# Optimization experiments

Hardware: AMD Instinct MI355X
Metric: run time of the kernel (lower is better)

## Reference

```python
import jax, jax.numpy as jnp
import numpy as np

T, H_IN = 2048, 84
HID = 256
NA = 18


def _conv(x, w, b, stride):
    # x: [N,C,H,W], w: [O,I,kh,kw]
    y = jax.lax.conv_general_dilated(
        x, w, window_strides=(stride, stride), padding='VALID',
        dimension_numbers=('NCHW', 'OIHW', 'NCHW'))
    return jax.nn.relu(y + b[None, :, None, None])


def setup_inputs() -> dict:
    key = jax.random.key(0)
    ks = jax.random.split(key, 17)
    p = lambda k, shape, s=0.05: (jax.random.normal(k, shape, jnp.float32) * s)
    return {
        'input_frames': jax.random.uniform(ks[0], (T, 1, H_IN, H_IN), jnp.float32),
        'conv1_w': p(ks[1], (32, 1, 8, 8)),   'conv1_b': p(ks[2], (32,)),
        'conv2_w': p(ks[3], (64, 32, 4, 4)),  'conv2_b': p(ks[4], (64,)),
        'conv3_w': p(ks[5], (256, 64, 3, 3)), 'conv3_b': p(ks[6], (256,)),
        'attn_w1': p(ks[7], (HID, HID)),      'attn_b1': p(ks[8], (HID,)),
        'attn_w2': p(ks[9], (HID, HID)),      'attn_b2': p(ks[10], (HID,)),
        'lstm_w_ih': p(ks[11], (4 * HID, HID)), 'lstm_w_hh': p(ks[12], (4 * HID, HID)),
        'lstm_b_ih': p(ks[13], (4 * HID,)),     'lstm_b_hh': p(ks[14], (4 * HID,)),
        'q_w': p(ks[15], (NA, HID)),          'q_b': p(ks[16], (NA,)),
    }


def reference(input_frames, conv1_w, conv1_b, conv2_w, conv2_b, conv3_w, conv3_b,
              attn_w1, attn_b1, attn_w2, attn_b2,
              lstm_w_ih, lstm_w_hh, lstm_b_ih, lstm_b_hh, q_w, q_b):
    # CNN over all frames at once (loop in torch was over frames; math identical)
    x = _conv(input_frames, conv1_w, conv1_b, 4)   # [T,32,20,20]
    x = _conv(x, conv2_w, conv2_b, 2)              # [T,64,9,9]
    fm = _conv(x, conv3_w, conv3_b, 1)             # [T,256,7,7]
    t, c, hh, ww = fm.shape
    # build_vector: vectors[i, ch] = fm[ch, y, x], i = y*W + x
    vecs = fm.reshape(t, c, hh * ww).transpose(0, 2, 1)  # [T,49,256]

    def step(carry, v):
        h, cc = carry  # [256], [256]
        # additive attention; softmax over the 256 feature dim per spatial vector
        s = jnp.tanh(v @ attn_w1.T + attn_b1 + h)              # [49,256]
        w = jax.nn.softmax(s @ attn_w2.T + attn_b2, axis=-1)   # [49,256]
        ctx = jnp.sum(w * v, axis=0)                           # [256]
        # single-layer LSTM cell, torch gate order i,f,g,o
        gates = ctx @ lstm_w_ih.T + lstm_b_ih + h @ lstm_w_hh.T + lstm_b_hh
        i, f, g, o = jnp.split(gates, 4)
        c_new = jax.nn.sigmoid(f) * cc + jax.nn.sigmoid(i) * jnp.tanh(g)
        h_new = jax.nn.sigmoid(o) * jnp.tanh(c_new)
        return (h_new, c_new), None

    h0 = jnp.zeros((HID,), fm.dtype)
    (h_T, _), _ = jax.lax.scan(step, (h0, h0), vecs)
    q = h_T @ q_w.T + q_b          # [18]
    return q[None, :]              # [1, nr_actions], matches torch output
```

## Files before the change

kernel.cpp:

```cpp
#include <hip/hip_runtime.h>
#include <hip/hip_bf16.h>
#include <math.h>


#define T_FRAMES 2048
#define NI 49
#define HID 256
#define NA 18
#define NWG 8

typedef __bf16 v8bf __attribute__((ext_vector_type(8)));
typedef float v4f __attribute__((ext_vector_type(4)));

static constexpr size_t OFF_FM1   = 0;
static constexpr size_t OFF_FM2   = 104857600;
static constexpr size_t OFF_VECS  = 147324928;
static constexpr size_t OFF_W2B   = 250085376;
static constexpr size_t OFF_WIHB  = OFF_W2B  + 131072;
static constexpr size_t OFF_WHHB  = OFF_WIHB + 524288;
static constexpr size_t OFF_W1T   = OFF_WHHB + 524288;
static constexpr size_t OFF_HBUF  = OFF_FM2;
static constexpr size_t OFF_CPUB  = OFF_FM2 + 2048;

__global__ void prep_weights(const float* __restrict__ w2, const float* __restrict__ wih,
                             const float* __restrict__ whh, const float* __restrict__ w1,
                             __bf16* w2b, __bf16* wihb, __bf16* whhb, float* w1t) {
  int idx = blockIdx.x * 256 + threadIdx.x;
  int stride = gridDim.x * 256;
  for (int i = idx; i < 65536; i += stride) w2b[i] = (__bf16)w2[i];
  for (int i = idx; i < 262144; i += stride) wihb[i] = (__bf16)wih[i];
  for (int i = idx; i < 262144; i += stride) whhb[i] = (__bf16)whh[i];
  for (int i = idx; i < 65536; i += stride) {
    int r = i >> 8, c = i & 255;
    w1t[c * 256 + r] = w1[i];
  }
}

__global__ void conv1_k(const float* __restrict__ x, const float* __restrict__ w,
                        const float* __restrict__ b, float* __restrict__ y) {
  int idx = blockIdx.x * 256 + threadIdx.x;
  if (idx >= T_FRAMES * 32 * 20 * 20) return;
  int xx = idx % 20, yy = (idx / 20) % 20, o = (idx / 400) % 32, t = idx / 12800;
  const float* xp = x + t * 7056 + yy * 4 * 84 + xx * 4;
  const float* wp = w + o * 64;
  float acc = b[o];
  #pragma unroll
  for (int ky = 0; ky < 8; ky++)
    #pragma unroll
    for (int kx = 0; kx < 8; kx++)
      acc += xp[ky * 84 + kx] * wp[ky * 8 + kx];
  y[idx] = fmaxf(acc, 0.f);
}

__global__ __launch_bounds__(256) void conv2_k(const float* __restrict__ fm1, const float* __restrict__ w,
                                               const float* __restrict__ b, float* __restrict__ fm2) {
  __shared__ float xs[32 * 400];
  int t = blockIdx.x, tid = threadIdx.x;
  for (int i = tid; i < 12800; i += 256) xs[i] = fm1[t * 12800 + i];
  __syncthreads();
  int o = tid >> 2, q = tid & 3;
  int p0 = q * 21, p1 = (p0 + 21 < 81) ? p0 + 21 : 81;
  int ob[21];
  #pragma unroll
  for (int i2 = 0; i2 < 21; i2++) {
    int p = p0 + i2; if (p > 80) p = 80;
    int yy = p / 9, xx2 = p - yy * 9;
    ob[i2] = yy * 40 + xx2 * 2;
  }
  float acc[21];
  #pragma unroll
  for (int i2 = 0; i2 < 21; i2++) acc[i2] = 0.f;
  for (int c = 0; c < 32; c++) {
    int cbase = c * 400;
    for (int ky = 0; ky < 4; ky++)
      for (int kx = 0; kx < 4; kx++) {
        float wgt = w[((o * 32 + c) * 4 + ky) * 4 + kx];
        int kyo = ky * 20 + kx;
        #pragma unroll
        for (int i2 = 0; i2 < 21; i2++)
          acc[i2] += wgt * xs[cbase + ob[i2] + kyo];
      }
  }
  float bo = b[o];
  #pragma unroll
  for (int i2 = 0; i2 < 21; i2++) {
    int p = p0 + i2;
    if (p < p1) fm2[t * 5184 + o * 81 + p] = fmaxf(acc[i2] + bo, 0.f);
  }
}

__global__ __launch_bounds__(256) void conv3_k(const float* __restrict__ fm2, const float* __restrict__ w,
                                               const float* __restrict__ b, float* __restrict__ vecs) {
  __shared__ float xs[64 * 81];
  __shared__ float ws4[256][37];
  int t = blockIdx.x, tid = threadIdx.x;
  for (int i = tid; i < 64 * 81; i += 256) xs[i] = fm2[t * 5184 + i];
  float acc[49];
  #pragma unroll
  for (int i = 0; i < 49; i++) acc[i] = 0.f;
  for (int c0 = 0; c0 < 64; c0 += 4) {
    __syncthreads();
    for (int i = tid; i < 256 * 36; i += 256) {
      int oo = i / 36, j = i - oo * 36;
      ws4[oo][j] = w[oo * 576 + c0 * 9 + j];
    }
    __syncthreads();
    for (int cc = 0; cc < 4; cc++)
      for (int ky = 0; ky < 3; ky++)
        for (int kx = 0; kx < 3; kx++) {
          float wgt = ws4[tid][cc * 9 + ky * 3 + kx];
          const float* xp = &xs[(c0 + cc) * 81 + ky * 9 + kx];
          #pragma unroll
          for (int yy = 0; yy < 7; yy++)
            #pragma unroll
            for (int xx = 0; xx < 7; xx++)
              acc[yy * 7 + xx] += wgt * xp[yy * 9 + xx];
        }
  }
  float bo = b[tid];
  for (int i = 0; i < 49; i++)
    vecs[(t * 49 + i) * 256 + tid] = fmaxf(acc[i] + bo, 0.f);
}

__global__ __launch_bounds__(256) void aprep_k(const float* __restrict__ vecs, const float* __restrict__ w1t,
                                               const float* __restrict__ b1, float* __restrict__ A) {
  __shared__ float vs[49][256];
  int t = blockIdx.x, tid = threadIdx.x;
  for (int i = tid; i < 49 * 256; i += 256) vs[i >> 8][i & 255] = vecs[t * 12544 + i];
  __syncthreads();
  float acc[49];
  #pragma unroll
  for (int i = 0; i < 49; i++) acc[i] = 0.f;
  for (int k = 0; k < 256; k++) {
    float wgt = w1t[k * 256 + tid];
    #pragma unroll
    for (int i = 0; i < 49; i++) acc[i] += vs[i][k] * wgt;
  }
  float bb = b1[tid];
  for (int i = 0; i < 49; i++) A[(t * 49 + i) * 256 + tid] = acc[i] + bb;
}

__global__ void init_comm(unsigned long long* hbuf, unsigned long long* cpub) {
  int idx = blockIdx.x * 256 + threadIdx.x;
  if (idx < 256) hbuf[idx] = 0ull;
  if (idx < NWG * 128) cpub[idx] = 0ull;
}

__device__ __forceinline__ float tanh_fast(float x) {
  float e = __expf(2.f * x);
  return 1.f - 2.f * __builtin_amdgcn_rcpf(e + 1.f);
}
__device__ __forceinline__ float sigm_fast(float x) {
  return __builtin_amdgcn_rcpf(1.f + __expf(-x));
}

__global__ __launch_bounds__(256, 1) void scan_k(
    const float* __restrict__ A, const float* __restrict__ vecs,
    const __bf16* __restrict__ w2b, const __bf16* __restrict__ wihb, const __bf16* __restrict__ whhb,
    const float* __restrict__ b2g, const float* __restrict__ bihg, const float* __restrict__ bhhg,
    const float* __restrict__ qw, const float* __restrict__ qb,
    unsigned long long* hbuf, unsigned long long* cpub, float* out) {
  if (blockIdx.x & 7) return;
  const int w = blockIdx.x >> 3;

  __shared__ __bf16 Ss[16][264];
  __shared__ float hs[HID];
  __shared__ __bf16 hbf[HID];
  __shared__ float Wt[8][HID];
  __shared__ float cxp[8][HID];
  __shared__ float b2s[HID];
  __shared__ float gb[4][32];
  __shared__ unsigned cpl[128];

  const int tid = threadIdx.x;
  const int lane = tid & 63;
  const int wv = tid >> 6;
  const int quad = lane >> 4;
  const int l15 = lane & 15;
  const int r0 = 6 * w;
  const int nr = (w < 7) ? 6 : 7;
  const int prow = tid >> 5;
  const int pcol = (tid & 31) * 8;

  for (int i = tid; i < 16 * 264; i += 256) (&Ss[0][0])[i] = (__bf16)0.f;
  for (int i = tid; i < 8 * HID; i += 256) (&cxp[0][0])[i] = 0.f;
  b2s[tid] = b2g[tid];
  hs[tid] = 0.f;
  hbf[tid] = (__bf16)0.f;
  float cbias[4];
  if (tid < 32) {
    #pragma unroll
    for (int g = 0; g < 4; g++) {
      int row = 256 * g + 32 * w + tid;
      cbias[g] = bihg[row] + bhhg[row];
    }
  }
  float creg = 0.f;

  v8bf BW2[4][8];
  #pragma unroll
  for (int ntl = 0; ntl < 4; ntl++) {
    const int row = wv * 64 + ntl * 16 + l15;
    #pragma unroll
    for (int k = 0; k < 8; k++)
      BW2[ntl][k] = *(const v8bf*)(w2b + row * 256 + k * 32 + quad * 8);
  }
  v8bf BIH[2][8], BHH[2][8];
  #pragma unroll
  for (int nt = 0; nt < 2; nt++) {
    const int row = 256 * wv + 32 * w + nt * 16 + l15;
    #pragma unroll
    for (int k = 0; k < 8; k++) {
      BIH[nt][k] = *(const v8bf*)(wihb + row * 256 + k * 32 + quad * 8);
      BHH[nt][k] = *(const v8bf*)(whhb + row * 256 + k * 32 + quad * 8);
    }
  }
  __syncthreads();

  for (int t = 0; t < T_FRAMES; t++) {
    int rr = r0 + prow; if (rr > 48) rr = 48;
    const float* Ap = A + ((long)t * NI + rr) * HID + pcol;
    const float* Vp = vecs + ((long)t * NI + rr) * HID + pcol;
    const float4 a40 = *(const float4*)(Ap);
    const float4 a41 = *(const float4*)(Ap + 4);
    const float4 v40 = *(const float4*)(Vp);
    const float4 v41 = *(const float4*)(Vp + 4);

    if (t > 0) {
      const unsigned tgt = (unsigned)t;
      unsigned long long pk =
          __hip_atomic_load(&hbuf[tid], __ATOMIC_RELAXED, __HIP_MEMORY_SCOPE_AGENT);
      int guard = 0;
      while ((unsigned)(pk >> 32) < tgt && ++guard < 5000000) {
        __builtin_amdgcn_s_sleep(1);
        pk = __hip_atomic_load(&hbuf[tid], __ATOMIC_RELAXED, __HIP_MEMORY_SCOPE_AGENT);
      }
      float hv = __uint_as_float((unsigned)pk);
      hs[tid] = hv;
      hbf[tid] = (__bf16)hv;
      __syncthreads();
    }

    if (prow < nr) {
      const float* hp = &hs[pcol];
      v8bf sv;
      sv[0] = (__bf16)tanh_fast(a40.x + hp[0]);
      sv[1] = (__bf16)tanh_fast(a40.y + hp[1]);
      sv[2] = (__bf16)tanh_fast(a40.z + hp[2]);
      sv[3] = (__bf16)tanh_fast(a40.w + hp[3]);
      sv[4] = (__bf16)tanh_fast(a41.x + hp[4]);
      sv[5] = (__bf16)tanh_fast(a41.y + hp[5]);
      sv[6] = (__bf16)tanh_fast(a41.z + hp[6]);
      sv[7] = (__bf16)tanh_fast(a41.w + hp[7]);
      *(v8bf*)&Ss[prow][pcol] = sv;
    }
    __syncthreads();

    v4f acc[4];
    #pragma unroll
    for (int ntl = 0; ntl < 4; ntl++) acc[ntl] = (v4f){0.f, 0.f, 0.f, 0.f};
    #pragma unroll
    for (int k = 0; k < 8; k++) {
      const v8bf av = *(const v8bf*)&Ss[l15][k * 32 + quad * 8];
      #pragma unroll
      for (int ntl = 0; ntl < 4; ntl++)
        acc[ntl] = __builtin_amdgcn_mfma_f32_16x16x32_bf16(av, BW2[ntl][k], acc[ntl], 0, 0, 0);
    }
    if (quad < 2) {
      #pragma unroll
      for (int ntl = 0; ntl < 4; ntl++) {
        const int col = wv * 64 + ntl * 16 + l15;
        const float bb = b2s[col];
        #pragma unroll
        for (int reg = 0; reg < 4; reg++)
          Wt[quad * 4 + reg][col] = acc[ntl][reg] + bb;
      }
    }
    __syncthreads();

    if (prow < nr) {
      float x[8];
      *(float4*)&x[0] = *(const float4*)&Wt[prow][pcol];
      *(float4*)&x[4] = *(const float4*)&Wt[prow][pcol + 4];
      float m = x[0];
      #pragma unroll
      for (int i = 1; i < 8; i++) m = fmaxf(m, x[i]);
      #pragma unroll
      for (int off = 16; off; off >>= 1) m = fmaxf(m, __shfl_xor(m, off, 64));
      float e[8], sm = 0.f;
      #pragma unroll
      for (int i = 0; i < 8; i++) { e[i] = __expf(x[i] - m); sm += e[i]; }
      #pragma unroll
      for (int off = 16; off; off >>= 1) sm += __shfl_xor(sm, off, 64);
      const float inv = __builtin_amdgcn_rcpf(sm);
      cxp[prow][pcol + 0] = e[0] * inv * v40.x;
      cxp[prow][pcol + 1] = e[1] * inv * v40.y;
      cxp[prow][pcol + 2] = e[2] * inv * v40.z;
      cxp[prow][pcol + 3] = e[3] * inv * v40.w;
      cxp[prow][pcol + 4] = e[4] * inv * v41.x;
      cxp[prow][pcol + 5] = e[5] * inv * v41.y;
      cxp[prow][pcol + 6] = e[6] * inv * v41.z;
      cxp[prow][pcol + 7] = e[7] * inv * v41.w;
    }
    __syncthreads();

    float cp = 0.f;
    #pragma unroll
    for (int r = 0; r < 8; r++) cp += cxp[r][tid];
    float cpo = __shfl_xor(cp, 1, 64);
    unsigned word = 0u;
    if ((tid & 1) == 0) {
      union { __bf16 b; unsigned short s; } lo, hi;
      lo.b = (__bf16)cp; hi.b = (__bf16)cpo;
      word = ((unsigned)hi.s << 16) | (unsigned)lo.s;
      unsigned long long pk =
          ((unsigned long long)(unsigned)(t + 1) << 32) | (unsigned long long)word;
      __hip_atomic_store(&cpub[w * 128 + (tid >> 1)], pk, __ATOMIC_RELAXED, __HIP_MEMORY_SCOPE_AGENT);
      cpl[tid >> 1] = word;
    }
    __syncthreads();

    unsigned long long g[8][4];
    const unsigned ctgt = (unsigned)(t + 1);
    const bool remote = (l15 < NWG) && (l15 != w);
    if (remote) {
      const unsigned long long* src = cpub + l15 * 128 + quad * 4;
      #pragma unroll
      for (int k = 0; k < 8; k++)
        #pragma unroll
        for (int q2 = 0; q2 < 4; q2++)
          g[k][q2] = __hip_atomic_load(&src[k * 16 + q2], __ATOMIC_RELAXED, __HIP_MEMORY_SCOPE_AGENT);
    }

    v4f gacc[2];
    gacc[0] = (v4f){0.f, 0.f, 0.f, 0.f};
    gacc[1] = (v4f){0.f, 0.f, 0.f, 0.f};
    #pragma unroll
    for (int k = 0; k < 8; k++) {
      v8bf hf;
      #pragma unroll
      for (int z = 0; z < 8; z++) hf[z] = (__bf16)0.f;
      if (l15 == 0) hf = *(const v8bf*)&hbf[k * 32 + quad * 8];
      gacc[0] = __builtin_amdgcn_mfma_f32_16x16x32_bf16(hf, BHH[0][k], gacc[0], 0, 0, 0);
      gacc[1] = __builtin_amdgcn_mfma_f32_16x16x32_bf16(hf, BHH[1][k], gacc[1], 0, 0, 0);
    }

    {
      bool ok = true;
      if (remote) {
        #pragma unroll
        for (int k = 0; k < 8; k++)
          #pragma unroll
          for (int q2 = 0; q2 < 4; q2++)
            ok &= ((unsigned)(g[k][q2] >> 32) >= ctgt);
      }
      if (!__all(ok)) {
        int guard = 0;
        while (true) {
          __builtin_amdgcn_s_sleep(1);
          ok = true;
          if (remote) {
            const unsigned long long* src = cpub + l15 * 128 + quad * 4;
            #pragma unroll
            for (int k = 0; k < 8; k++)
              #pragma unroll
              for (int q2 = 0; q2 < 4; q2++) {
                g[k][q2] = __hip_atomic_load(&src[k * 16 + q2], __ATOMIC_RELAXED, __HIP_MEMORY_SCOPE_AGENT);
                ok &= ((unsigned)(g[k][q2] >> 32) >= ctgt);
              }
          }
          if (__all(ok) || ++guard > 5000000) break;
        }
      }
    }

    #pragma unroll
    for (int k = 0; k < 8; k++) {
      union { unsigned u[4]; v8bf v; } pf;
      if (remote) {
        pf.u[0] = (unsigned)g[k][0]; pf.u[1] = (unsigned)g[k][1];
        pf.u[2] = (unsigned)g[k][2]; pf.u[3] = (unsigned)g[k][3];
      } else if (l15 == w) {
        pf.u[0] = cpl[k * 16 + quad * 4 + 0];
        pf.u[1] = cpl[k * 16 + quad * 4 + 1];
        pf.u[2] = cpl[k * 16 + quad * 4 + 2];
        pf.u[3] = cpl[k * 16 + quad * 4 + 3];
      } else {
        pf.u[0] = pf.u[1] = pf.u[2] = pf.u[3] = 0u;
      }
      gacc[0] = __builtin_amdgcn_mfma_f32_16x16x32_bf16(pf.v, BIH[0][k], gacc[0], 0, 0, 0);
      gacc[1] = __builtin_amdgcn_mfma_f32_16x16x32_bf16(pf.v, BIH[1][k], gacc[1], 0, 0, 0);
    }
    #pragma unroll
    for (int nt = 0; nt < 2; nt++) {
      float tot = gacc[nt][0] + gacc[nt][1] + gacc[nt][2] + gacc[nt][3];
      tot += __shfl_xor(tot, 16, 64);
      tot += __shfl_xor(tot, 32, 64);
      if (lane < 16) gb[wv][nt * 16 + lane] = tot;
    }
    __syncthreads();

    if (tid < 32) {
      float gi = gb[0][tid] + cbias[0];
      float gf = gb[1][tid] + cbias[1];
      float gg = gb[2][tid] + cbias[2];
      float go = gb[3][tid] + cbias[3];
      float si = sigm_fast(gi);
      float sf = sigm_fast(gf);
      float so = sigm_fast(go);
      creg = sf * creg + si * tanh_fast(gg);
      float hn = so * tanh_fast(creg);
      unsigned long long pk = ((unsigned long long)(unsigned)(t + 1) << 32) |
                              (unsigned long long)__float_as_uint(hn);
      __hip_atomic_store(&hbuf[32 * w + tid], pk, __ATOMIC_RELAXED, __HIP_MEMORY_SCOPE_AGENT);
    }
  }

  if (w == 0) {
    const unsigned tgt = (unsigned)T_FRAMES;
    unsigned long long pk =
        __hip_atomic_load(&hbuf[tid], __ATOMIC_RELAXED, __HIP_MEMORY_SCOPE_AGENT);
    int guard = 0;
    while ((unsigned)(pk >> 32) < tgt && ++guard < 5000000) {
      __builtin_amdgcn_s_sleep(1);
      pk = __hip_atomic_load(&hbuf[tid], __ATOMIC_RELAXED, __HIP_MEMORY_SCOPE_AGENT);
    }
    hs[tid] = __uint_as_float((unsigned)pk);
    __syncthreads();
    if (tid < NA) {
      float acc = qb[tid];
      for (int k = 0; k < HID; k++) acc += hs[k] * qw[tid * HID + k];
      out[tid] = acc;
    }
  }
}

extern "C" void kernel_launch(void* const* d_in, const int* in_sizes, int n_in,
                              void* d_out, int out_size, void* d_ws, size_t ws_size,
                              hipStream_t stream) {
  const float* frames = (const float*)d_in[0];
  const float* c1w = (const float*)d_in[1];
  const float* c1b = (const float*)d_in[2];
  const float* c2w = (const float*)d_in[3];
  const float* c2b = (const float*)d_in[4];
  const float* c3w = (const float*)d_in[5];
  const float* c3b = (const float*)d_in[6];
  const float* aw1 = (const float*)d_in[7];
  const float* ab1 = (const float*)d_in[8];
  const float* aw2 = (const float*)d_in[9];
  const float* ab2 = (const float*)d_in[10];
  const float* wih = (const float*)d_in[11];
  const float* whh = (const float*)d_in[12];
  const float* bih = (const float*)d_in[13];
  const float* bhh = (const float*)d_in[14];
  const float* qw  = (const float*)d_in[15];
  const float* qb  = (const float*)d_in[16];

  char* ws = (char*)d_ws;
  float*  fm1   = (float*)(ws + OFF_FM1);
  float*  A     = (float*)(ws + OFF_FM1);
  float*  fm2   = (float*)(ws + OFF_FM2);
  float*  vecs  = (float*)(ws + OFF_VECS);
  __bf16* w2b   = (__bf16*)(ws + OFF_W2B);
  __bf16* wihb  = (__bf16*)(ws + OFF_WIHB);
  __bf16* whhb  = (__bf16*)(ws + OFF_WHHB);
  float*  w1t   = (float*)(ws + OFF_W1T);
  unsigned long long* hbuf = (unsigned long long*)(ws + OFF_HBUF);
  unsigned long long* cpub = (unsigned long long*)(ws + OFF_CPUB);

  prep_weights<<<256, 256, 0, stream>>>(aw2, wih, whh, aw1, w2b, wihb, whhb, w1t);
  conv1_k<<<102400, 256, 0, stream>>>(frames, c1w, c1b, fm1);
  conv2_k<<<T_FRAMES, 256, 0, stream>>>(fm1, c2w, c2b, fm2);
  conv3_k<<<T_FRAMES, 256, 0, stream>>>(fm2, c3w, c3b, vecs);
  aprep_k<<<T_FRAMES, 256, 0, stream>>>(vecs, w1t, ab1, A);
  init_comm<<<4, 256, 0, stream>>>(hbuf, cpub);
  scan_k<<<57, 256, 0, stream>>>(A, vecs, w2b, wihb, whhb, ab2, bih, bhh, qw, qb,
                                 hbuf, cpub, (float*)d_out);
}
```

Before: 17.37 ms.

## Add sc0 fast-path polling for cross-workgroup LSTM handoff with fallback

```diff
diff --git a/kernel.cpp b/kernel.cpp
--- a/kernel.cpp
+++ b/kernel.cpp
@@ -19,8 +19,8 @@
 static constexpr size_t OFF_WIHB  = OFF_W2B  + 131072;
 static constexpr size_t OFF_WHHB  = OFF_WIHB + 524288;
 static constexpr size_t OFF_W1T   = OFF_WHHB + 524288;
-static constexpr size_t OFF_HBUF  = OFF_FM2;
-static constexpr size_t OFF_CPUB  = OFF_FM2 + 2048;
+static constexpr size_t OFF_COMM  = OFF_FM2;
+static constexpr unsigned long long MAGICC = 0xC0FFEE5EED123400ull;
 
 __global__ void prep_weights(const float* __restrict__ w2, const float* __restrict__ wih,
                              const float* __restrict__ whh, const float* __restrict__ w1,
@@ -140,10 +140,10 @@
   for (int i = 0; i < 49; i++) A[(t * 49 + i) * 256 + tid] = acc[i] + bb;
 }
 
-__global__ void init_comm(unsigned long long* hbuf, unsigned long long* cpub) {
+__global__ void init_comm(unsigned long long* comm) {
   int idx = blockIdx.x * 256 + threadIdx.x;
-  if (idx < 256) hbuf[idx] = 0ull;
-  if (idx < NWG * 128) cpub[idx] = 0ull;
+  if (idx < 1408)
+    __hip_atomic_store(&comm[idx], 0ull, __ATOMIC_RELAXED, __HIP_MEMORY_SCOPE_AGENT);
 }
 
 __device__ __forceinline__ float tanh_fast(float x) {
@@ -152,6 +152,16 @@
 }
 __device__ __forceinline__ float sigm_fast(float x) {
   return __builtin_amdgcn_rcpf(1.f + __expf(-x));
+}
+
+__device__ __forceinline__ void st_u64_sc0(unsigned long long* p, unsigned long long v) {
+  asm volatile("global_store_dwordx2 %0, %1, off sc0" :: "v"(p), "v"(v) : "memory");
+}
+__device__ __forceinline__ unsigned long long ld_u64_sc0(const unsigned long long* p) {
+  unsigned long long v;
+  asm volatile("global_load_dwordx2 %0, %1, off sc0\n\ts_waitcnt vmcnt(0)"
+               : "=v"(v) : "v"(p) : "memory");
+  return v;
 }
 
 __global__ __launch_bounds__(256, 1) void scan_k(
@@ -159,9 +169,13 @@
     const __bf16* __restrict__ w2b, const __bf16* __restrict__ wihb, const __bf16* __restrict__ whhb,
     const float* __restrict__ b2g, const float* __restrict__ bihg, const float* __restrict__ bhhg,
     const float* __restrict__ qw, const float* __restrict__ qb,
-    unsigned long long* hbuf, unsigned long long* cpub, float* out) {
+    unsigned long long* comm, float* out) {
   if (blockIdx.x & 7) return;
   const int w = blockIdx.x >> 3;
+
+  unsigned long long* hbuf  = comm;
+  unsigned long long* cpub  = comm + 256;
+  unsigned long long* probe = comm + 1280;
 
   __shared__ __bf16 Ss[16][264];
   __shared__ float hs[HID];
@@ -171,6 +185,9 @@
   __shared__ float b2s[HID];
   __shared__ float gb[4][32];
   __shared__ unsigned cpl[128];
+  __shared__ int fastsh;
+  __shared__ int expired;
+  __shared__ int demotes;
 
   const int tid = threadIdx.x;
   const int lane = tid & 63;
@@ -182,6 +199,8 @@
   const int prow = tid >> 5;
   const int pcol = (tid & 31) * 8;
 
+  if (tid == 0) st_u64_sc0(&probe[w * 16], MAGICC ^ (unsigned long long)w);
+
   for (int i = tid; i < 16 * 264; i += 256) (&Ss[0][0])[i] = (__bf16)0.f;
   for (int i = tid; i < 8 * HID; i += 256) (&cxp[0][0])[i] = 0.f;
   b2s[tid] = b2g[tid];
@@ -214,6 +233,17 @@
       BIH[nt][k] = *(const v8bf*)(wihb + row * 256 + k * 32 + quad * 8);
       BHH[nt][k] = *(const v8bf*)(whhb + row * 256 + k * 32 + quad * 8);
     }
+  }
+
+  if (wv == 0) {
+    bool ok = false;
+    int gd = 0;
+    while (!ok && ++gd < 3000) {
+      unsigned long long v = (lane < 8) ? ld_u64_sc0(&probe[lane * 16]) : 0ull;
+      bool mine = (lane < 8) ? (v == (MAGICC ^ (unsigned long long)lane)) : true;
+      ok = __all(mine);
+    }
+    if (tid == 0) { fastsh = ok ? 1 : 0; expired = 0; demotes = 0; }
   }
   __syncthreads();
 
@@ -228,12 +258,23 @@
 
     if (t > 0) {
       const unsigned tgt = (unsigned)t;
-      unsigned long long pk =
-          __hip_atomic_load(&hbuf[tid], __ATOMIC_RELAXED, __HIP_MEMORY_SCOPE_AGENT);
-      int guard = 0;
-      while ((unsigned)(pk >> 32) < tgt && ++guard < 5000000) {
-        __builtin_amdgcn_s_sleep(1);
+      unsigned long long pk = 0;
+      bool got = false;
+      if (fastsh) {
+        int gd = 0;
+        do {
+          pk = ld_u64_sc0(&hbuf[tid]);
+          got = ((unsigned)(pk >> 32) == tgt);
+        } while (!got && ++gd < 8000);
+        if (!got) expired = 1;
+      }
+      if (!got) {
         pk = __hip_atomic_load(&hbuf[tid], __ATOMIC_RELAXED, __HIP_MEMORY_SCOPE_AGENT);
+        int gd = 0;
+        while ((unsigned)(pk >> 32) != tgt && ++gd < 5000000) {
+          __builtin_amdgcn_s_sleep(1);
+          pk = __hip_atomic_load(&hbuf[tid], __ATOMIC_RELAXED, __HIP_MEMORY_SCOPE_AGENT);
+        }
       }
       float hv = __uint_as_float((unsigned)pk);
       hs[tid] = hv;
@@ -308,29 +349,17 @@
     #pragma unroll
     for (int r = 0; r < 8; r++) cp += cxp[r][tid];
     float cpo = __shfl_xor(cp, 1, 64);
-    unsigned word = 0u;
     if ((tid & 1) == 0) {
       union { __bf16 b; unsigned short s; } lo, hi;
       lo.b = (__bf16)cp; hi.b = (__bf16)cpo;
-      word = ((unsigned)hi.s << 16) | (unsigned)lo.s;
+      unsigned word = ((unsigned)hi.s << 16) | (unsigned)lo.s;
       unsigned long long pk =
           ((unsigned long long)(unsigned)(t + 1) << 32) | (unsigned long long)word;
+      st_u64_sc0(&cpub[w * 128 + (tid >> 1)], pk);
       __hip_atomic_store(&cpub[w * 128 + (tid >> 1)], pk, __ATOMIC_RELAXED, __HIP_MEMORY_SCOPE_AGENT);
       cpl[tid >> 1] = word;
     }
     __syncthreads();
-
-    unsigned long long g[8][4];
-    const unsigned ctgt = (unsigned)(t + 1);
-    const bool remote = (l15 < NWG) && (l15 != w);
-    if (remote) {
-      const unsigned long long* src = cpub + l15 * 128 + quad * 4;
-      #pragma unroll
-      for (int k = 0; k < 8; k++)
-        #pragma unroll
-        for (int q2 = 0; q2 < 4; q2++)
-          g[k][q2] = __hip_atomic_load(&src[k * 16 + q2], __ATOMIC_RELAXED, __HIP_MEMORY_SCOPE_AGENT);
-    }
 
     v4f gacc[2];
     gacc[0] = (v4f){0.f, 0.f, 0.f, 0.f};
@@ -345,32 +374,55 @@
       gacc[1] = __builtin_amdgcn_mfma_f32_16x16x32_bf16(hf, BHH[1][k], gacc[1], 0, 0, 0);
     }
 
-    {
-      bool ok = true;
-      if (remote) {
-        #pragma unroll
-        for (int k = 0; k < 8; k++)
+    unsigned long long g[8][4];
+    const unsigned ctgt = (unsigned)(t + 1);
+    const bool remote = (l15 < NWG) && (l15 != w);
+    bool got = false;
+    if (fastsh) {
+      int gd = 0;
+      while (!got && ++gd < 4000) {
+        bool ok = true;
+        if (remote) {
+          const unsigned long long* src = cpub + l15 * 128 + quad * 4;
+#define G_LD(K,Q,IMM) asm volatile("global_load_dwordx2 %0, %1, off offset:" #IMM " sc0" \
+                                   : "=v"(g[K][Q]) : "v"(src))
+          G_LD(0,0,0);   G_LD(0,1,8);   G_LD(0,2,16);  G_LD(0,3,24);
+          G_LD(1,0,128); G_LD(1,1,136); G_LD(1,2,144); G_LD(1,3,152);
+          G_LD(2,0,256); G_LD(2,1,264); G_LD(2,2,272); G_LD(2,3,280);
+          G_LD(3,0,384); G_LD(3,1,392); G_LD(3,2,400); G_LD(3,3,408);
+          G_LD(4,0,512); G_LD(4,1,520); G_LD(4,2,528); G_LD(4,3,536);
+          G_LD(5,0,640); G_LD(5,1,648); G_LD(5,2,656); G_LD(5,3,664);
+          G_LD(6,0,768); G_LD(6,1,776); G_LD(6,2,784); G_LD(6,3,792);
+          G_LD(7,0,896); G_LD(7,1,904); G_LD(7,2,912); G_LD(7,3,920);
+#undef G_LD
+          asm volatile("s_waitcnt vmcnt(0)" ::: "memory");
+          __builtin_amdgcn_sched_barrier(0);
           #pragma unroll
-          for (int q2 = 0; q2 < 4; q2++)
-            ok &= ((unsigned)(g[k][q2] >> 32) >= ctgt);
-      }
-      if (!__all(ok)) {
-        int guard = 0;
-        while (true) {
-          __builtin_amdgcn_s_sleep(1);
-          ok = true;
-          if (remote) {
-            const unsigned long long* src = cpub + l15 * 128 + quad * 4;
+          for (int k = 0; k < 8; k++)
             #pragma unroll
-            for (int k = 0; k < 8; k++)
-              #pragma unroll
-              for (int q2 = 0; q2 < 4; q2++) {
-                g[k][q2] = __hip_atomic_load(&src[k * 16 + q2], __ATOMIC_RELAXED, __HIP_MEMORY_SCOPE_AGENT);
-                ok &= ((unsigned)(g[k][q2] >> 32) >= ctgt);
-              }
-          }
-          if (__all(ok) || ++guard > 5000000) break;
+            for (int q2 = 0; q2 < 4; q2++)
+              ok &= ((unsigned)(g[k][q2] >> 32) == ctgt);
         }
+        got = __all(ok);
+      }
+      if (!got) expired = 1;
+    }
+    if (!got) {
+      int gd = 0;
+      while (true) {
+        bool ok = true;
+        if (remote) {
+          const unsigned long long* src = cpub + l15 * 128 + quad * 4;
+          #pragma unroll
+          for (int k = 0; k < 8; k++)
+            #pragma unroll
+            for (int q2 = 0; q2 < 4; q2++) {
+              g[k][q2] = __hip_atomic_load(&src[k * 16 + q2], __ATOMIC_RELAXED, __HIP_MEMORY_SCOPE_AGENT);
+              ok &= ((unsigned)(g[k][q2] >> 32) == ctgt);
+            }
+        }
+        if (__all(ok) || ++gd > 5000000) break;
+        __builtin_amdgcn_s_sleep(1);
       }
     }
 
@@ -400,6 +452,11 @@
     }
     __syncthreads();
 
+    if (tid == 0 && expired) {
+      expired = 0;
+      if (++demotes >= 3) fastsh = 0;
+    }
+
     if (tid < 32) {
       float gi = gb[0][tid] + cbias[0];
       float gf = gb[1][tid] + cbias[1];
@@ -412,6 +469,7 @@
       float hn = so * tanh_fast(creg);
       unsigned long long pk = ((unsigned long long)(unsigned)(t + 1) << 32) |
                               (unsigned long long)__float_as_uint(hn);
+      st_u64_sc0(&hbuf[32 * w + tid], pk);
       __hip_atomic_store(&hbuf[32 * w + tid], pk, __ATOMIC_RELAXED, __HIP_MEMORY_SCOPE_AGENT);
     }
   }
@@ -420,8 +478,8 @@
     const unsigned tgt = (unsigned)T_FRAMES;
     unsigned long long pk =
         __hip_atomic_load(&hbuf[tid], __ATOMIC_RELAXED, __HIP_MEMORY_SCOPE_AGENT);
-    int guard = 0;
-    while ((unsigned)(pk >> 32) < tgt && ++guard < 5000000) {
+    int gd = 0;
+    while ((unsigned)(pk >> 32) != tgt && ++gd < 5000000) {
       __builtin_amdgcn_s_sleep(1);
       pk = __hip_atomic_load(&hbuf[tid], __ATOMIC_RELAXED, __HIP_MEMORY_SCOPE_AGENT);
     }
@@ -465,15 +523,14 @@
   __bf16* wihb  = (__bf16*)(ws + OFF_WIHB);
   __bf16* whhb  = (__bf16*)(ws + OFF_WHHB);
   float*  w1t   = (float*)(ws + OFF_W1T);
-  unsigned long long* hbuf = (unsigned long long*)(ws + OFF_HBUF);
-  unsigned long long* cpub = (unsigned long long*)(ws + OFF_CPUB);
+  unsigned long long* comm = (unsigned long long*)(ws + OFF_COMM);
 
   prep_weights<<<256, 256, 0, stream>>>(aw2, wih, whh, aw1, w2b, wihb, whhb, w1t);
   conv1_k<<<102400, 256, 0, stream>>>(frames, c1w, c1b, fm1);
   conv2_k<<<T_FRAMES, 256, 0, stream>>>(fm1, c2w, c2b, fm2);
   conv3_k<<<T_FRAMES, 256, 0, stream>>>(fm2, c3w, c3b, vecs);
   aprep_k<<<T_FRAMES, 256, 0, stream>>>(vecs, w1t, ab1, A);
-  init_comm<<<4, 256, 0, stream>>>(hbuf, cpub);
+  init_comm<<<6, 256, 0, stream>>>(comm);
   scan_k<<<57, 256, 0, stream>>>(A, vecs, w2b, wihb, whhb, ab2, bih, bhh, qw, qb,
-                                 hbuf, cpub, (float*)d_out);
-}
+                                 comm, (float*)d_out);
+}
```

New measurement: 39.91 ms. 130% more time.
